# Performance work log

Hardware: AMD Instinct MI355X
Metric: run time of the kernel (lower is better)

The kernel has to match this reference:

```python
import jax, jax.numpy as jnp
import numpy as np

B, S, T = 8, 128, 24          # batch, src_len, max_len (enc_len = 2*S)
V, E, H = 32000, 512, 512     # vocab, embed_dim, hidden_dim
D = 3 * H + E                 # pointer-head feature dim = 2*dec_hid + emb + enc_hid


def setup_inputs() -> dict:
    key = jax.random.key(0)
    ks = jax.random.split(key, 25)
    def u(k, shape, scale):
        return jax.random.uniform(k, shape, jnp.float32, -scale, scale)
    s_h = 1.0 / np.sqrt(H).astype(np.float32)
    s_d = 1.0 / np.sqrt(D).astype(np.float32)
    s_2h = 1.0 / np.sqrt(2 * H).astype(np.float32)
    return {
        'pre_seq': jax.random.randint(ks[0], (B, S), 0, V),
        'post_seq': jax.random.randint(ks[1], (B, S), 0, V),
        'trg': jax.random.randint(ks[2], (B, T), 0, V),
        'emb': jax.random.normal(ks[3], (V, E), jnp.float32) * 0.02,
        'Wih_pre': u(ks[4], (3 * H, E), s_h), 'Whh_pre': u(ks[5], (3 * H, H), s_h),
        'bih_pre': u(ks[6], (3 * H,), s_h), 'bhh_pre': u(ks[7], (3 * H,), s_h),
        'Wih_post': u(ks[8], (3 * H, E), s_h), 'Whh_post': u(ks[9], (3 * H, H), s_h),
        'bih_post': u(ks[10], (3 * H,), s_h), 'bhh_post': u(ks[11], (3 * H,), s_h),
        'fc_enc_W': u(ks[12], (H, 2 * H), s_2h), 'fc_enc_b': u(ks[13], (H,), s_2h),
        'attn_W': u(ks[14], (H, 2 * H), s_2h), 'attn_b': u(ks[15], (H,), s_2h),
        'attn_v': u(ks[16], (1, H), s_h),
        'Wih_dec': u(ks[17], (3 * H, H + E), s_h), 'Whh_dec': u(ks[18], (3 * H, H), s_h),
        'bih_dec': u(ks[19], (3 * H,), s_h), 'bhh_dec': u(ks[20], (3 * H,), s_h),
        'fc_hid_W': u(ks[21], (D, D), s_d), 'fc_hid_b': u(ks[22], (D,), s_d),
        'fc_out_W': u(ks[23], (1, D), s_d), 'fc_out_b': u(ks[24], (1,), s_d),
    }


def gru_cell(x, h, Wih, Whh, bih, bhh):
    # torch GRU gate order: reset, update, new
    gi = x @ Wih.T + bih
    gh = h @ Whh.T + bhh
    ir, iz, inn = jnp.split(gi, 3, axis=-1)
    hr, hz, hn = jnp.split(gh, 3, axis=-1)
    r = jax.nn.sigmoid(ir + hr)
    z = jax.nn.sigmoid(iz + hz)
    n = jnp.tanh(inn + r * hn)
    return (1.0 - z) * n + z * h


def run_gru(x_seq, Wih, Whh, bih, bhh):
    # x_seq: [B, L, E] -> outputs [B, L, H], last hidden [B, H]
    h0 = jnp.zeros((x_seq.shape[0], Whh.shape[1]), x_seq.dtype)
    def step(h, x):
        h2 = gru_cell(x, h, Wih, Whh, bih, bhh)
        return h2, h2
    h_last, ys = jax.lax.scan(step, h0, jnp.swapaxes(x_seq, 0, 1))
    return jnp.swapaxes(ys, 0, 1), h_last


def reference(pre_seq, post_seq, trg, emb,
              Wih_pre, Whh_pre, bih_pre, bhh_pre,
              Wih_post, Whh_post, bih_post, bhh_post,
              fc_enc_W, fc_enc_b, attn_W, attn_b, attn_v,
              Wih_dec, Whh_dec, bih_dec, bhh_dec,
              fc_hid_W, fc_hid_b, fc_out_W, fc_out_b):
    bsz, src_len = pre_seq.shape
    # ---- Encoder (dropout in eval mode = identity) ----
    pre_out, pre_h = run_gru(emb[pre_seq], Wih_pre, Whh_pre, bih_pre, bhh_pre)
    post_out, post_h = run_gru(emb[post_seq], Wih_post, Whh_post, bih_post, bhh_post)
    enc_out = jnp.concatenate([pre_out, post_out], axis=1)          # [B, 2S, H]
    hidden = jnp.tanh(jnp.concatenate([pre_h, post_h], axis=-1) @ fc_enc_W.T + fc_enc_b)
    # ---- Attention: split attn_W into hidden- and encoder- parts (cat order: hidden, enc) ----
    W_hid, W_enc = attn_W[:, :H], attn_W[:, H:]
    enc_proj = jnp.einsum('blh,dh->bld', enc_out, W_enc) + attn_b   # step-invariant [B, L, H]
    L = enc_out.shape[1]
    # decoder input tokens: pre_seq[:, -1] then trg[:, :-1] (always teacher forced)
    tokens = jnp.concatenate([pre_seq[:, -1:], trg[:, :-1]], axis=1)  # [B, T]

    def dec_step(h, tok):
        e = emb[tok]                                                # [B, E]
        energy = jnp.tanh(enc_proj + (h @ W_hid.T)[:, None, :])     # [B, L, H]
        scores = jnp.einsum('blh,h->bl', energy, attn_v[0])
        a = jax.nn.softmax(scores, axis=1)                          # [B, L]
        weighted = jnp.einsum('bl,blh->bh', a, enc_out)             # [B, H]
        h2 = gru_cell(jnp.concatenate([e, weighted], axis=-1), h,
                      Wih_dec, Whh_dec, bih_dec, bhh_dec)           # [B, H]
        feats = jnp.concatenate([
            enc_out,
            jnp.broadcast_to(weighted[:, None, :], (bsz, L, H)),
            jnp.broadcast_to(h2[:, None, :], (bsz, L, H)),
            jnp.broadcast_to(e[:, None, :], (bsz, L, E)),
        ], axis=-1)                                                 # [B, L, 3H+E]
        hid = feats @ fc_hid_W.T + fc_hid_b                         # [B, L, D]
        logits = (hid @ fc_out_W.T + fc_out_b)[..., 0]              # [B, L]
        return h2, logits

    _, ys = jax.lax.scan(dec_step, hidden, tokens.T)                # [T, B, L]
    outs = jnp.swapaxes(ys, 0, 1)                                   # [B, T, L]
    return outs[:, :, :src_len], outs[:, :, src_len:]
```

## Files before the change

kernel.cpp:

```cpp
#include <hip/hip_runtime.h>
#include <cstdint>

#define B_ 8
#define S_ 128
#define T_ 24
#define E_ 512
#define H_ 512
#define H3_ 1536
#define L_ 256
#define D_ 2048

typedef unsigned long long u64;

__device__ __forceinline__ float fsig(float x) { return 1.0f / (1.0f + __expf(-x)); }
__device__ __forceinline__ float ftanh(float x) { return 1.0f - 2.0f / (1.0f + __expf(2.0f * x)); }
__device__ __forceinline__ float dot4(float4 a, float4 b) {
    return a.x * b.x + a.y * b.y + a.z * b.z + a.w * b.w;
}

__device__ __forceinline__ u64 cohLoadU64(const u64* p) {
    return __hip_atomic_load((u64*)p, __ATOMIC_RELAXED, __HIP_MEMORY_SCOPE_AGENT);
}
__device__ __forceinline__ void cohStoreU64(u64* p, u64 v) {
    __hip_atomic_store(p, v, __ATOMIC_RELAXED, __HIP_MEMORY_SCOPE_AGENT);
}
__device__ __forceinline__ float2 asF2(u64 v) { union { u64 u; float2 f; } x; x.u = v; return x.f; }
__device__ __forceinline__ u64 packF2(float v, float tag) { union { float2 f; u64 u; } x; x.f = make_float2(v, tag); return x.u; }

__global__ void k_boot(const int* __restrict__ pre, const int* __restrict__ post,
                       const int* __restrict__ trg,
                       int* __restrict__ idxPre, int* __restrict__ idxPost,
                       int* __restrict__ idxTok, float* __restrict__ wEff,
                       u64* __restrict__ clr, int n) {
    int gtid = blockIdx.x * 256 + threadIdx.x;
    for (int i = gtid; i < n; i += gridDim.x * 256) clr[i] = 0ull;
    if (gtid < 1024) {
        int s = gtid >> 3, b = gtid & 7;
        idxPre[gtid]  = pre[b * S_ + s];
        idxPost[gtid] = post[b * S_ + s];
    }
    if (gtid < T_ * B_) {
        int t = gtid >> 3, b = gtid & 7;
        idxTok[gtid] = (t == 0) ? pre[b * S_ + (S_ - 1)] : trg[b * T_ + (t - 1)];
    }
    if (gtid < 2048) wEff[gtid] = 0.f;
}

__device__ void gemm_body(
    const float* __restrict__ A, const int* __restrict__ Aidx, int lda,
    const float* __restrict__ Bm, int ldb,
    const float* __restrict__ bias, float* __restrict__ C,
    int N, int K, int gbx, int gby) {
    __shared__ float As[16][68];
    __shared__ float Bs[16][68];
    const int m0 = gbx * 64, n0 = gby * 64;
    const int tid = threadIdx.x;
    const int tm = tid >> 2;
    const int tk = (tid & 3) << 2;
    const int tx = tid & 15, ty = tid >> 4;
    const int am = m0 + tm;
    const float* Arow = A + (size_t)(Aidx ? Aidx[am] : am) * lda;
    const float* Brow = Bm + (size_t)(n0 + tm) * ldb;
    float acc[4][4] = {};
    for (int k0 = 0; k0 < K; k0 += 16) {
        float4 av = *(const float4*)(Arow + k0 + tk);
        float4 bv = *(const float4*)(Brow + k0 + tk);
        __syncthreads();
        As[tk][tm] = av.x; As[tk + 1][tm] = av.y; As[tk + 2][tm] = av.z; As[tk + 3][tm] = av.w;
        Bs[tk][tm] = bv.x; Bs[tk + 1][tm] = bv.y; Bs[tk + 2][tm] = bv.z; Bs[tk + 3][tm] = bv.w;
        __syncthreads();
#pragma unroll
        for (int k = 0; k < 16; ++k) {
            float4 a4 = *(const float4*)(&As[k][ty << 2]);
            float4 b4 = *(const float4*)(&Bs[k][tx << 2]);
            float ar[4] = {a4.x, a4.y, a4.z, a4.w};
            float br[4] = {b4.x, b4.y, b4.z, b4.w};
#pragma unroll
            for (int i = 0; i < 4; ++i)
#pragma unroll
                for (int j = 0; j < 4; ++j) acc[i][j] += ar[i] * br[j];
        }
    }
    float4 bb = bias ? *(const float4*)(bias + n0 + (tx << 2)) : make_float4(0.f, 0.f, 0.f, 0.f);
#pragma unroll
    for (int i = 0; i < 4; ++i) {
        int m = m0 + (ty << 2) + i;
        float4 o;
        o.x = acc[i][0] + bb.x; o.y = acc[i][1] + bb.y;
        o.z = acc[i][2] + bb.z; o.w = acc[i][3] + bb.w;
        *(float4*)(C + (size_t)m * N + n0 + (tx << 2)) = o;
    }
}

__global__ __launch_bounds__(256) void k_mid(
    const float* __restrict__ emb, const int* __restrict__ idxTok,
    const float* __restrict__ WihDec, const float* __restrict__ bihDec, float* __restrict__ giE,
    const float* __restrict__ encOut, const float* __restrict__ attnW,
    const float* __restrict__ attnB, float* __restrict__ encProj,
    const float* __restrict__ fcHidW, const float* __restrict__ fcHidB,
    const float* __restrict__ fcOutW, const float* __restrict__ fcOutB,
    float* __restrict__ wEff, float* __restrict__ bEff,
    const float* __restrict__ fcEncW, const float* __restrict__ fcEncB,
    float* __restrict__ hBuf) {
    const int bx = blockIdx.x;
    const int tid = threadIdx.x;
    if (bx < 72) {
        gemm_body(emb, idxTok, 512, WihDec, 1024, bihDec, giE, 1536, 512, bx % 3, bx / 3);
    } else if (bx < 328) {
        int r = bx - 72;
        gemm_body(encOut, nullptr, 512, attnW + 512, 1024, attnB, encProj, 512, 512, r & 31, r >> 5);
    } else if (bx < 457) {
        __shared__ float red[256];
        int wb = bx - 328;
        if (wb < 128) {
            int cblk = wb & 7, q = wb >> 3;
            int col = cblk * 256 + tid;
            int j0 = q * 128;
            float acc = 0.f;
            for (int j = j0; j < j0 + 128; ++j) acc += fcOutW[j] * fcHidW[(size_t)j * D_ + col];
            atomicAdd(wEff + col, acc);
        } else {
            float p = 0.f;
            for (int j = tid; j < D_; j += 256) p += fcOutW[j] * fcHidB[j];
            red[tid] = p;
            __syncthreads();
            for (int s = 128; s > 0; s >>= 1) {
                if (tid < s) red[tid] += red[tid + s];
                __syncthreads();
            }
            if (tid == 0) bEff[0] = red[0] + fcOutB[0];
        }
    } else {
        int o = (bx - 457) * 256 + tid;
        int b = o >> 9, j = o & 511;
        const float4* w4 = (const float4*)(fcEncW + (size_t)j * 1024);
        const float4* pre4 = (const float4*)(encOut + (((size_t)(b << 8) + 127) << 9));
        const float4* post4 = (const float4*)(encOut + (((size_t)(b << 8) + 255) << 9));
        float acc = fcEncB[j];
        for (int k = 0; k < 128; ++k) acc += dot4(w4[k], pre4[k]);
        for (int k = 0; k < 128; ++k) acc += dot4(w4[128 + k], post4[k]);
        hBuf[o] = ftanh(acc);
    }
}

__global__ __launch_bounds__(512, 2) void k_encoder(
    const float* __restrict__ emb, const int* __restrict__ idxPre, const int* __restrict__ idxPost,
    const float* __restrict__ WihPre, const float* __restrict__ WihPost,
    const float* __restrict__ bihPre, const float* __restrict__ bihPost,
    const float* __restrict__ WhhPre, const float* __restrict__ WhhPost,
    const float* __restrict__ bhhPre, const float* __restrict__ bhhPost,
    float* __restrict__ encOut, u64* __restrict__ encEx) {
    const int bx = blockIdx.x;
    const int chain = bx >> 4;
    const int p = bx & 15;
    const int gr = chain >> 3, b = chain & 7;
    const int kb = p << 5;
    const int tid = threadIdx.x;
    const int c = tid >> 4, l = tid & 15;
    const int j = kb + c;
    const float* Wih = gr ? WihPost : WihPre;
    const float* bih = gr ? bihPost : bihPre;
    const float* Whh = gr ? WhhPost : WhhPre;
    const float* bhh = gr ? bhhPost : bhhPre;
    const int* idx = gr ? idxPost : idxPre;
    u64* ex0 = encEx + chain * 512;

    __shared__ float hS[576];
    __shared__ float eS[576];

    float wr[32], wz[32], wn[32], ur[32], uz[32], un[32];
    {
        const float* r0 = Whh + (size_t)j * 512 + l * 32;
        const float* r1 = r0 + 512 * 512;
        const float* r2 = r1 + 512 * 512;
        const float* u0 = Wih + (size_t)j * 512 + l * 32;
        const float* u1 = u0 + 512 * 512;
        const float* u2 = u1 + 512 * 512;
#pragma unroll
        for (int m = 0; m < 32; ++m) {
            wr[m] = r0[m]; wz[m] = r1[m]; wn[m] = r2[m];
            ur[m] = u0[m]; uz[m] = u1[m]; un[m] = u2[m];
        }
    }
    const float b0 = bih[j] + bhh[j];
    const float b1 = bih[512 + j] + bhh[512 + j];
    const float bi2 = bih[1024 + j];
    const float bh2 = bhh[1024 + j];

    for (int t = 0; t < S_; ++t) {
        int tok = idx[t * 8 + b];
        float ev = emb[(size_t)tok * 512 + tid];
        if (t == 0) {
            hS[(tid >> 5) * 36 + (tid & 31)] = 0.f;
        } else {
            const float tag = (float)t;
            const u64* src = ex0 + (t & 1) * 8192;
            float v;
            for (;;) {
                float2 f = asF2(cohLoadU64(src + tid));
                if (f.y == tag) { v = f.x; break; }
                __builtin_amdgcn_s_sleep(1);
            }
            hS[(tid >> 5) * 36 + (tid & 31)] = v;
        }
        eS[(tid >> 5) * 36 + (tid & 31)] = ev;
        __syncthreads();
        const float* hseg = hS + l * 36;
        const float* eseg = eS + l * 36;
        float a0 = 0.f, a1 = 0.f, a2h = 0.f, a2i = 0.f;
#pragma unroll
        for (int m = 0; m < 32; ++m) {
            float hv = hseg[m], evv = eseg[m];
            a0 += wr[m] * hv + ur[m] * evv;
            a1 += wz[m] * hv + uz[m] * evv;
            a2h += wn[m] * hv;
            a2i += un[m] * evv;
        }
#pragma unroll
        for (int off = 8; off; off >>= 1) {
            a0 += __shfl_xor(a0, off, 16);
            a1 += __shfl_xor(a1, off, 16);
            a2h += __shfl_xor(a2h, off, 16);
            a2i += __shfl_xor(a2i, off, 16);
        }
        if (l == 0) {
            float r = fsig(a0 + b0);
            float z = fsig(a1 + b1);
            float n = ftanh(a2i + bi2 + r * (a2h + bh2));
            float h2 = (1.f - z) * n + z * hS[p * 36 + c];
            cohStoreU64(ex0 + ((t + 1) & 1) * 8192 + j, packF2(h2, (float)(t + 1)));
            encOut[(((size_t)(b << 8) + (gr << 7) + t) << 9) + j] = h2;
        }
        __syncthreads();
    }
}

__global__ __launch_bounds__(512, 2) void k_decoder(
    const float* __restrict__ encOut, const float* __restrict__ encProj,
    const float* __restrict__ attnW, const float* __restrict__ attnV,
    const float* __restrict__ WihDec, const float* __restrict__ WhhDec,
    const float* __restrict__ bhhDec, const float* __restrict__ giE,
    const float* __restrict__ wEff, const float* __restrict__ hBuf,
    const float* __restrict__ emb, const int* __restrict__ idxTok,
    u64* __restrict__ hEx, u64* __restrict__ hpP,
    u64* __restrict__ scEx, u64* __restrict__ wtEx,
    float* __restrict__ cpart, float* __restrict__ encDot, float* __restrict__ eDot4) {
    const int tid = threadIdx.x;
    const int bx = blockIdx.x;
    __shared__ float shm[9664];

    if (bx < 32) {
        const int g = bx;
        const int s = tid >> 5, kq = tid & 31;
        const int j = (g << 4) + s;
        float wr[16], wz[16], wn[16], vr[16], vz[16], vn[16], ap[16];
#pragma unroll
        for (int m = 0; m < 16; ++m) {
            int k = kq + 32 * m;
            wr[m] = WhhDec[(size_t)j * 512 + k];
            wz[m] = WhhDec[(size_t)(512 + j) * 512 + k];
            wn[m] = WhhDec[(size_t)(1024 + j) * 512 + k];
            vr[m] = WihDec[(size_t)j * 1024 + 512 + k];
            vz[m] = WihDec[(size_t)(512 + j) * 1024 + 512 + k];
            vn[m] = WihDec[(size_t)(1024 + j) * 1024 + 512 + k];
            ap[m] = attnW[(size_t)tid * 1024 + (g << 4) + m];
        }
        float* hL = shm;
        float* xL = shm + 4096;
        float* mS = shm + 8192;
        if (tid < 128) { int ss = tid >> 3, bb = tid & 7; mS[1152 + tid] = hBuf[(bb << 9) + (g << 4) + ss]; }
        if (tid < 48) mS[1280 + tid] = bhhDec[(tid >> 4) * 512 + (g << 4) + (tid & 15)];
        __syncthreads();
        {
            u64* hdst = hpP + (size_t)g * 4096;
#pragma unroll
            for (int bb = 0; bb < 8; ++bb) {
                float acch = 0.f;
#pragma unroll
                for (int m = 0; m < 16; ++m) acch += ap[m] * mS[1152 + m * 8 + bb];
                cohStoreU64(hdst + bb * 512 + tid, packF2(acch, 1.0f));
            }
        }
        for (int t = 0; t < T_; ++t) {
            const int par = t & 1;
            const float tagi = (float)(t + 1);
            if (t == 0) {
#pragma unroll
                for (int i = 0; i < 8; ++i) hL[tid + 512 * i] = hBuf[tid + 512 * i];
            } else {
                const float tagh = (float)t;
                const u64* src = hEx + par * 4096;
                float v[8];
                for (;;) {
                    u64 rr[8]; bool ok = true;
#pragma unroll
                    for (int i = 0; i < 8; ++i) rr[i] = cohLoadU64(src + tid + 512 * i);
#pragma unroll
                    for (int i = 0; i < 8; ++i) { float2 f = asF2(rr[i]); v[i] = f.x; ok &= (f.y == tagh); }
                    if (ok) break;
                    __builtin_amdgcn_s_sleep(1);
                }
#pragma unroll
                for (int i = 0; i < 8; ++i) hL[tid + 512 * i] = v[i];
            }
            __syncthreads();
            for (int bb = 0; bb < 8; ++bb) {
                const float* hb = hL + (bb << 9);
                float ar = 0.f, az = 0.f, an = 0.f;
#pragma unroll
                for (int m = 0; m < 16; ++m) {
                    float hv = hb[kq + 32 * m];
                    ar += wr[m] * hv; az += wz[m] * hv; an += wn[m] * hv;
                }
#pragma unroll
                for (int off = 16; off; off >>= 1) {
                    ar += __shfl_xor(ar, off); az += __shfl_xor(az, off); an += __shfl_xor(an, off);
                }
                if (kq == 0) {
                    mS[s * 8 + bb]       = ar;
                    mS[128 + s * 8 + bb] = az;
                    mS[256 + s * 8 + bb] = an;
                }
            }
            if (tid < 384) {
                int bb = tid / 48, idx2 = tid % 48, g3 = idx2 >> 4, ss = idx2 & 15;
                mS[768 + g3 * 128 + ss * 8 + bb] =
                    giE[((size_t)(t << 3) + bb) * H3_ + g3 * 512 + (g << 4) + ss];
            }
            {
                const u64* src = wtEx + par * 4096;
                float v[8];
                for (;;) {
                    u64 rr[8]; bool ok = true;
#pragma unroll
                    for (int i = 0; i < 8; ++i) rr[i] = cohLoadU64(src + tid + 512 * i);
#pragma unroll
                    for (int i = 0; i < 8; ++i) { float2 f = asF2(rr[i]); v[i] = f.x; ok &= (f.y == tagi); }
                    if (ok) break;
                    __builtin_amdgcn_s_sleep(1);
                }
#pragma unroll
                for (int i = 0; i < 8; ++i) xL[tid + 512 * i] = v[i];
            }
            __syncthreads();
            for (int bb = 0; bb < 8; ++bb) {
                const float* wb = xL + (bb << 9);
                float ar = 0.f, az = 0.f, an = 0.f;
#pragma unroll
                for (int m = 0; m < 16; ++m) {
                    float wv = wb[kq + 32 * m];
                    ar += vr[m] * wv; az += vz[m] * wv; an += vn[m] * wv;
                }
#pragma unroll
                for (int off = 16; off; off >>= 1) {
                    ar += __shfl_xor(ar, off); az += __shfl_xor(az, off); an += __shfl_xor(an, off);
                }
                if (kq == 0) {
                    mS[384 + s * 8 + bb] = ar;
                    mS[512 + s * 8 + bb] = az;
                    mS[640 + s * 8 + bb] = an;
                }
            }
            __syncthreads();
            if (tid < 128) {
                int ss = tid >> 3, bb = tid & 7;
                int jj = (g << 4) + ss;
                int o = ss * 8 + bb;
                float ghr = mS[o]       + mS[1280 + ss];
                float ghz = mS[128 + o] + mS[1296 + ss];
                float ghn = mS[256 + o] + mS[1312 + ss];
                float gir = mS[384 + o] + mS[768 + o];
                float giz = mS[512 + o] + mS[896 + o];
                float gin = mS[640 + o] + mS[1024 + o];
                float r = fsig(gir + ghr), z = fsig(giz + ghz);
                float n = ftanh(gin + r * ghn);
                float h2 = (1.f - z) * n + z * hL[(bb << 9) + jj];
                cohStoreU64(hEx + ((t + 1) & 1) * 4096 + (bb << 9) + jj, packF2(h2, (float)(t + 1)));
                mS[1152 + o] = h2;
                mS[1328 + o] = h2 * wEff[1024 + jj];
            }
            __syncthreads();
            if (tid < 8) {
                float pc = 0.f;
#pragma unroll
                for (int q = 0; q < 16; ++q) pc += mS[1328 + q * 8 + tid];
                cpart[(tid * T_ + t) * 48 + g] = pc;
            }
            if (t < T_ - 1) {
                const float tg = (float)(t + 2);
                u64* hdst = hpP + (size_t)((t + 1) & 1) * 131072 + (size_t)g * 4096;
#pragma unroll
                for (int bb = 0; bb < 8; ++bb) {
                    float acch = 0.f;
#pragma unroll
                    for (int m = 0; m < 16; ++m) acch += ap[m] * mS[1152 + m * 8 + bb];
                    cohStoreU64(hdst + bb * 512 + tid, packF2(acch, tg));
                }
            }
            __syncthreads();
        }
    } else if (bx < 96) {
        const int id = bx - 32;
        const int b = id >> 3, lq = id & 7;
        float* hpS = shm;
        float* vS  = shm + 512;
        vS[tid] = attnV[tid];
        __syncthreads();
        const int kq = tid & 63, lg = tid >> 6;
        for (int t = 0; t < T_; ++t) {
            const int par = t & 1;
            const float tagi = (float)(t + 1);
            {
                const u64* src = hpP + (size_t)par * 131072 + (size_t)b * 512 + tid;
                float sum;
                for (;;) {
                    bool ok = true; float s2 = 0.f;
                    u64 ra[16];
#pragma unroll
                    for (int pp = 0; pp < 16; ++pp) ra[pp] = cohLoadU64(src + (size_t)pp * 4096);
#pragma unroll
                    for (int pp = 0; pp < 16; ++pp) { float2 f = asF2(ra[pp]); s2 += f.x; ok &= (f.y == tagi); }
#pragma unroll
                    for (int pp = 0; pp < 16; ++pp) ra[pp] = cohLoadU64(src + (size_t)(16 + pp) * 4096);
#pragma unroll
                    for (int pp = 0; pp < 16; ++pp) { float2 f = asF2(ra[pp]); s2 += f.x; ok &= (f.y == tagi); }
                    if (ok) { sum = s2; break; }
                    __builtin_amdgcn_s_sleep(2);
                }
                hpS[tid] = sum;
            }
            __syncthreads();
            u64* dst = scEx + par * 2048 + (b << 8);
#pragma unroll
            for (int i = 0; i < 4; ++i) {
                int ll = lg + (i << 3);
                const float* ep = encProj + (((size_t)(b << 8) + (lq << 5) + ll) << 9);
                float sc = 0.f;
#pragma unroll
                for (int m = 0; m < 8; ++m) {
                    int k = kq + (m << 6);
                    sc += vS[k] * ftanh(ep[k] + hpS[k]);
                }
#pragma unroll
                for (int off = 32; off; off >>= 1) sc += __shfl_xor(sc, off);
                if (kq == 0) cohStoreU64(dst + (lq << 5) + ll, packF2(sc, tagi));
            }
            __syncthreads();
        }
    } else if (bx < 160) {
        const int id = bx - 96;
        const int b = id >> 3, cq = id & 7;
        const int c = tid & 63, lg = tid >> 6;
        float* aS = shm;
        float* rS = shm + 256;
        float* wS = shm + 288;
        float* lp = shm + 800;
        for (int t = 0; t < T_; ++t) {
            const int par = t & 1;
            const float tagi = (float)(t + 1);
            float sc = 0.f;
            if (tid < 256) {
                const u64* src = scEx + par * 2048 + (b << 8) + tid;
                for (;;) {
                    float2 f = asF2(cohLoadU64(src));
                    if (f.y == tagi) { sc = f.x; break; }
                    __builtin_amdgcn_s_sleep(1);
                }
            }
            float m = (tid < 256) ? sc : -1e30f;
#pragma unroll
            for (int off = 32; off; off >>= 1) m = fmaxf(m, __shfl_xor(m, off));
            if ((tid & 63) == 0) rS[tid >> 6] = m;
            __syncthreads();
            float mx = fmaxf(fmaxf(rS[0], rS[1]), fmaxf(rS[2], rS[3]));
            float e = (tid < 256) ? __expf(sc - mx) : 0.f;
            float ssum = e;
#pragma unroll
            for (int off = 32; off; off >>= 1) ssum += __shfl_xor(ssum, off);
            if ((tid & 63) == 0) rS[8 + (tid >> 6)] = ssum;
            if (tid < 256) aS[tid] = e;
            __syncthreads();
            float inv = 1.f / (rS[8] + rS[9] + rS[10] + rS[11]);
            float acc = 0.f;
#pragma unroll
            for (int mm = 0; mm < 32; ++mm) {
                int l = lg + (mm << 3);
                acc += aS[l] * encOut[(((size_t)(b << 8) + l) << 9) + (cq << 6) + c];
            }
            wS[lg * 64 + c] = acc;
            __syncthreads();
            if (tid < 64) {
                float wv = 0.f;
#pragma unroll
                for (int q = 0; q < 8; ++q) wv += wS[q * 64 + tid];
                wv *= inv;
                cohStoreU64(wtEx + par * 4096 + (b << 9) + (cq << 6) + tid, packF2(wv, tagi));
                lp[tid] = wv * wEff[512 + (cq << 6) + tid];
            }
            __syncthreads();
            if (tid == 0) {
                float pc = 0.f;
                for (int q = 0; q < 64; ++q) pc += lp[q];
                cpart[(b * T_ + t) * 48 + 32 + cq] = pc;
            }
            __syncthreads();
        }
    } else if (bx < 164) {
        int wid = tid >> 6, lane = tid & 63;
        int gw = (bx - 160) * 8 + wid;
        for (int o = gw; o < 2048; o += 32) {
            const float* row = encOut + ((size_t)o << 9);
            float s = 0.f;
            for (int k = lane; k < 512; k += 64) s += row[k] * wEff[k];
            for (int off = 32; off; off >>= 1) s += __shfl_down(s, off);
            if (lane == 0) encDot[o] = s;
        }
    } else {
        int wg = bx - 164;
        int o = wg * 8 + (tid >> 6);
        int lane = tid & 63;
        const float* row = emb + (size_t)idxTok[o] * E_;
        const float* w = wEff + 1536;
        float s = 0.f;
        for (int k = lane; k < 512; k += 64) s += row[k] * w[k];
        for (int off = 32; off; off >>= 1) s += __shfl_down(s, off);
        if (lane == 0) eDot4[o] = s;
    }
}

__global__ void k_csum(const float* __restrict__ cpart, const float* __restrict__ eDot4,
                       const float* __restrict__ bEff, float* __restrict__ cBuf) {
    int tid = threadIdx.x;
    if (tid < 192) {
        int b = tid / 24, t = tid % 24;
        float acc = eDot4[t * 8 + b] + bEff[0];
        const float* p = cpart + (b * T_ + t) * 48;
#pragma unroll
        for (int k = 0; k < 40; ++k) acc += p[k];
        cBuf[b * T_ + t] = acc;
    }
}

__global__ void k_final(const float* __restrict__ encDot, const float* __restrict__ c,
                        float* __restrict__ out) {
    int idx = blockIdx.x * 256 + threadIdx.x;
    const int half = B_ * T_ * S_;
    int w = idx < half ? idx : idx - half;
    int b = w / (T_ * S_);
    int r = w % (T_ * S_);
    int t = r / S_, sidx = r % S_;
    int l = (idx < half) ? sidx : (S_ + sidx);
    out[idx] = encDot[b * L_ + l] + c[b * T_ + t];
}

extern "C" void kernel_launch(void* const* d_in, const int* in_sizes, int n_in,
                              void* d_out, int out_size, void* d_ws, size_t ws_size,
                              hipStream_t stream) {
    const int* pre = (const int*)d_in[0];
    const int* post = (const int*)d_in[1];
    const int* trg = (const int*)d_in[2];
    const float* emb = (const float*)d_in[3];
    const float* WihPre = (const float*)d_in[4];
    const float* WhhPre = (const float*)d_in[5];
    const float* bihPre = (const float*)d_in[6];
    const float* bhhPre = (const float*)d_in[7];
    const float* WihPost = (const float*)d_in[8];
    const float* WhhPost = (const float*)d_in[9];
    const float* bihPost = (const float*)d_in[10];
    const float* bhhPost = (const float*)d_in[11];
    const float* fcEncW = (const float*)d_in[12];
    const float* fcEncB = (const float*)d_in[13];
    const float* attnW = (const float*)d_in[14];
    const float* attnB = (const float*)d_in[15];
    const float* attnV = (const float*)d_in[16];
    const float* WihDec = (const float*)d_in[17];
    const float* WhhDec = (const float*)d_in[18];
    const float* bihDec = (const float*)d_in[19];
    const float* bhhDec = (const float*)d_in[20];
    const float* fcHidW = (const float*)d_in[21];
    const float* fcHidB = (const float*)d_in[22];
    const float* fcOutW = (const float*)d_in[23];
    const float* fcOutB = (const float*)d_in[24];
    float* outp = (float*)d_out;

    float* base = (float*)d_ws;
    size_t off = 0;
    auto alloc = [&](size_t n) {
        float* p = base + off;
        off += (n + 63) & ~(size_t)63;
        return p;
    };
    float* giE = alloc(192 * 1536);
    float* encOut = alloc(8 * 256 * 512);
    float* encProj = alloc(8 * 256 * 512);
    float* wEff = alloc(2048);
    float* bEff = alloc(64);
    float* encDot = alloc(2048);
    float* eDot4 = alloc(256);
    float* hBuf = alloc(4096);
    float* cBuf = alloc(256);
    float* encExF = alloc(32768);
    float* hExF  = alloc(16384);
    float* hpPF  = alloc(524288);
    float* scExF = alloc(8192);
    float* wtExF = alloc(16384);
    float* cpart = alloc(8 * 24 * 48);
    int* idxPre = (int*)alloc(1024);
    int* idxPost = (int*)alloc(1024);
    int* idxTok = (int*)alloc(256);

    const int clearN = (32768 + 16384 + 524288 + 8192 + 16384) / 2;
    k_boot<<<512, 256, 0, stream>>>(pre, post, trg, idxPre, idxPost, idxTok, wEff,
                                    (u64*)encExF, clearN);
    k_encoder<<<256, 512, 0, stream>>>(emb, idxPre, idxPost, WihPre, WihPost,
                                       bihPre, bihPost, WhhPre, WhhPost,
                                       bhhPre, bhhPost, encOut, (u64*)encExF);
    k_mid<<<473, 256, 0, stream>>>(emb, idxTok, WihDec, bihDec, giE,
                                   encOut, attnW, attnB, encProj,
                                   fcHidW, fcHidB, fcOutW, fcOutB, wEff, bEff,
                                   fcEncW, fcEncB, hBuf);
    k_decoder<<<188, 512, 0, stream>>>(encOut, encProj, attnW, attnV,
                                       WihDec, WhhDec, bhhDec, giE, wEff, hBuf,
                                       emb, idxTok,
                                       (u64*)hExF, (u64*)hpPF, (u64*)scExF, (u64*)wtExF,
                                       cpart, encDot, eDot4);
    k_csum<<<1, 256, 0, stream>>>(cpart, eDot4, bEff, cBuf);
    k_final<<<192, 256, 0, stream>>>(encDot, cBuf, outp);
}
```

Measured before the change: 902.2 us.

## Replace per-element tagged exchanges with per-block flag counters in decoder

The decoder's cross-block exchanges for the hidden state, the attention-hidden projection partials and the weighted context used to pair every float with a step tag in 64-bit words. Consumers re-polled the whole buffer until every tag matched. Now the data is stored as plain floats, and each producer block publishes a single integer step counter after a block barrier. Consumers poll only the 32 or 64 counters, then read the data once. This halves exchange traffic and shrinks the boot-time buffer clearing. The catch is that correctness now relies on relaxed atomics plus workgroup barriers ordering data stores before flag stores, with no explicit release/acquire fences.

```diff
diff --git a/kernel.cpp b/kernel.cpp
--- a/kernel.cpp
+++ b/kernel.cpp
@@ -24,6 +24,18 @@
 __device__ __forceinline__ void cohStoreU64(u64* p, u64 v) {
     __hip_atomic_store(p, v, __ATOMIC_RELAXED, __HIP_MEMORY_SCOPE_AGENT);
 }
+__device__ __forceinline__ float cohLoadF(const float* p) {
+    return __hip_atomic_load((float*)p, __ATOMIC_RELAXED, __HIP_MEMORY_SCOPE_AGENT);
+}
+__device__ __forceinline__ void cohStoreF(float* p, float v) {
+    __hip_atomic_store(p, v, __ATOMIC_RELAXED, __HIP_MEMORY_SCOPE_AGENT);
+}
+__device__ __forceinline__ int cohLoadInt(const int* p) {
+    return __hip_atomic_load((int*)p, __ATOMIC_RELAXED, __HIP_MEMORY_SCOPE_AGENT);
+}
+__device__ __forceinline__ void cohStoreInt(int* p, int v) {
+    __hip_atomic_store(p, v, __ATOMIC_RELAXED, __HIP_MEMORY_SCOPE_AGENT);
+}
 __device__ __forceinline__ float2 asF2(u64 v) { union { u64 u; float2 f; } x; x.u = v; return x.f; }
 __device__ __forceinline__ u64 packF2(float v, float tag) { union { float2 f; u64 u; } x; x.f = make_float2(v, tag); return x.u; }
 
@@ -31,9 +43,10 @@
                        const int* __restrict__ trg,
                        int* __restrict__ idxPre, int* __restrict__ idxPost,
                        int* __restrict__ idxTok, float* __restrict__ wEff,
-                       u64* __restrict__ clr, int n) {
+                       u64* __restrict__ clr, int n, int* __restrict__ tags) {
     int gtid = blockIdx.x * 256 + threadIdx.x;
     for (int i = gtid; i < n; i += gridDim.x * 256) clr[i] = 0ull;
+    if (gtid < 128) tags[gtid] = 0;
     if (gtid < 1024) {
         int s = gtid >> 3, b = gtid & 7;
         idxPre[gtid]  = pre[b * S_ + s];
@@ -242,8 +255,9 @@
     const float* __restrict__ bhhDec, const float* __restrict__ giE,
     const float* __restrict__ wEff, const float* __restrict__ hBuf,
     const float* __restrict__ emb, const int* __restrict__ idxTok,
-    u64* __restrict__ hEx, u64* __restrict__ hpP,
-    u64* __restrict__ scEx, u64* __restrict__ wtEx,
+    float* __restrict__ hEx, float* __restrict__ hpD,
+    u64* __restrict__ scEx, float* __restrict__ wtEx,
+    int* __restrict__ gruTag, int* __restrict__ wtTag,
     float* __restrict__ cpart, float* __restrict__ encDot, float* __restrict__ eDot4) {
     const int tid = threadIdx.x;
     const int bx = blockIdx.x;
@@ -272,38 +286,37 @@
         if (tid < 48) mS[1280 + tid] = bhhDec[(tid >> 4) * 512 + (g << 4) + (tid & 15)];
         __syncthreads();
         {
-            u64* hdst = hpP + (size_t)g * 4096;
+            float* hdst = hpD + (size_t)g * 4096;
 #pragma unroll
             for (int bb = 0; bb < 8; ++bb) {
                 float acch = 0.f;
 #pragma unroll
                 for (int m = 0; m < 16; ++m) acch += ap[m] * mS[1152 + m * 8 + bb];
-                cohStoreU64(hdst + bb * 512 + tid, packF2(acch, 1.0f));
-            }
-        }
+                cohStoreF(hdst + bb * 512 + tid, acch);
+            }
+        }
+        __syncthreads();
+        if (tid == 0) cohStoreInt(gruTag + g, 1);
+
         for (int t = 0; t < T_; ++t) {
             const int par = t & 1;
-            const float tagi = (float)(t + 1);
             if (t == 0) {
 #pragma unroll
                 for (int i = 0; i < 8; ++i) hL[tid + 512 * i] = hBuf[tid + 512 * i];
+                __syncthreads();
             } else {
-                const float tagh = (float)t;
-                const u64* src = hEx + par * 4096;
-                float v[8];
+                const int want = t + 1;
                 for (;;) {
-                    u64 rr[8]; bool ok = true;
-#pragma unroll
-                    for (int i = 0; i < 8; ++i) rr[i] = cohLoadU64(src + tid + 512 * i);
-#pragma unroll
-                    for (int i = 0; i < 8; ++i) { float2 f = asF2(rr[i]); v[i] = f.x; ok &= (f.y == tagh); }
-                    if (ok) break;
-                    __builtin_amdgcn_s_sleep(1);
-                }
-#pragma unroll
-                for (int i = 0; i < 8; ++i) hL[tid + 512 * i] = v[i];
-            }
-            __syncthreads();
+                    int tg = want;
+                    if (tid < 32) tg = cohLoadInt(gruTag + tid);
+                    if (__syncthreads_and(tg >= want)) break;
+                    __builtin_amdgcn_s_sleep(2);
+                }
+                const float* src = hEx + par * 4096;
+#pragma unroll
+                for (int i = 0; i < 8; ++i) hL[tid + 512 * i] = cohLoadF(src + tid + 512 * i);
+                __syncthreads();
+            }
             for (int bb = 0; bb < 8; ++bb) {
                 const float* hb = hL + (bb << 9);
                 float ar = 0.f, az = 0.f, an = 0.f;
@@ -328,19 +341,16 @@
                     giE[((size_t)(t << 3) + bb) * H3_ + g3 * 512 + (g << 4) + ss];
             }
             {
-                const u64* src = wtEx + par * 4096;
-                float v[8];
+                const int want = t + 1;
                 for (;;) {
-                    u64 rr[8]; bool ok = true;
-#pragma unroll
-                    for (int i = 0; i < 8; ++i) rr[i] = cohLoadU64(src + tid + 512 * i);
-#pragma unroll
-                    for (int i = 0; i < 8; ++i) { float2 f = asF2(rr[i]); v[i] = f.x; ok &= (f.y == tagi); }
-                    if (ok) break;
-                    __builtin_amdgcn_s_sleep(1);
-                }
-#pragma unroll
-                for (int i = 0; i < 8; ++i) xL[tid + 512 * i] = v[i];
+                    int tg = want;
+                    if (tid < 64) tg = cohLoadInt(wtTag + tid);
+                    if (__syncthreads_and(tg >= want)) break;
+                    __builtin_amdgcn_s_sleep(2);
+                }
+                const float* src = wtEx + par * 4096;
+#pragma unroll
+                for (int i = 0; i < 8; ++i) xL[tid + 512 * i] = cohLoadF(src + tid + 512 * i);
             }
             __syncthreads();
             for (int bb = 0; bb < 8; ++bb) {
@@ -375,7 +385,7 @@
                 float r = fsig(gir + ghr), z = fsig(giz + ghz);
                 float n = ftanh(gin + r * ghn);
                 float h2 = (1.f - z) * n + z * hL[(bb << 9) + jj];
-                cohStoreU64(hEx + ((t + 1) & 1) * 4096 + (bb << 9) + jj, packF2(h2, (float)(t + 1)));
+                cohStoreF(hEx + ((t + 1) & 1) * 4096 + (bb << 9) + jj, h2);
                 mS[1152 + o] = h2;
                 mS[1328 + o] = h2 * wEff[1024 + jj];
             }
@@ -387,17 +397,17 @@
                 cpart[(tid * T_ + t) * 48 + g] = pc;
             }
             if (t < T_ - 1) {
-                const float tg = (float)(t + 2);
-                u64* hdst = hpP + (size_t)((t + 1) & 1) * 131072 + (size_t)g * 4096;
+                float* hdst = hpD + (size_t)((t + 1) & 1) * 131072 + (size_t)g * 4096;
 #pragma unroll
                 for (int bb = 0; bb < 8; ++bb) {
                     float acch = 0.f;
 #pragma unroll
                     for (int m = 0; m < 16; ++m) acch += ap[m] * mS[1152 + m * 8 + bb];
-                    cohStoreU64(hdst + bb * 512 + tid, packF2(acch, tg));
-                }
-            }
-            __syncthreads();
+                    cohStoreF(hdst + bb * 512 + tid, acch);
+                }
+                __syncthreads();
+                if (tid == 0) cohStoreInt(gruTag + g, t + 2);
+            }
         }
     } else if (bx < 96) {
         const int id = bx - 32;
@@ -411,22 +421,20 @@
             const int par = t & 1;
             const float tagi = (float)(t + 1);
             {
-                const u64* src = hpP + (size_t)par * 131072 + (size_t)b * 512 + tid;
-                float sum;
+                const int want = t + 1;
                 for (;;) {
-                    bool ok = true; float s2 = 0.f;
-                    u64 ra[16];
-#pragma unroll
-                    for (int pp = 0; pp < 16; ++pp) ra[pp] = cohLoadU64(src + (size_t)pp * 4096);
-#pragma unroll
-                    for (int pp = 0; pp < 16; ++pp) { float2 f = asF2(ra[pp]); s2 += f.x; ok &= (f.y == tagi); }
-#pragma unroll
-                    for (int pp = 0; pp < 16; ++pp) ra[pp] = cohLoadU64(src + (size_t)(16 + pp) * 4096);
-#pragma unroll
-                    for (int pp = 0; pp < 16; ++pp) { float2 f = asF2(ra[pp]); s2 += f.x; ok &= (f.y == tagi); }
-                    if (ok) { sum = s2; break; }
+                    int tg = want;
+                    if (tid < 32) tg = cohLoadInt(gruTag + tid);
+                    if (__syncthreads_and(tg >= want)) break;
                     __builtin_amdgcn_s_sleep(2);
                 }
+                const float* src = hpD + (size_t)par * 131072 + (size_t)b * 512 + tid;
+                float va[32];
+#pragma unroll
+                for (int g2 = 0; g2 < 32; ++g2) va[g2] = cohLoadF(src + (size_t)g2 * 4096);
+                float sum = 0.f;
+#pragma unroll
+                for (int g2 = 0; g2 < 32; ++g2) sum += va[g2];
                 hpS[tid] = sum;
             }
             __syncthreads();
@@ -494,11 +502,12 @@
 #pragma unroll
                 for (int q = 0; q < 8; ++q) wv += wS[q * 64 + tid];
                 wv *= inv;
-                cohStoreU64(wtEx + par * 4096 + (b << 9) + (cq << 6) + tid, packF2(wv, tagi));
+                cohStoreF(wtEx + par * 4096 + (b << 9) + (cq << 6) + tid, wv);
                 lp[tid] = wv * wEff[512 + (cq << 6) + tid];
             }
             __syncthreads();
             if (tid == 0) {
+                cohStoreInt(wtTag + (b << 3) + cq, t + 1);
                 float pc = 0.f;
                 for (int q = 0; q < 64; ++q) pc += lp[q];
                 cpart[(b * T_ + t) * 48 + 32 + cq] = pc;
@@ -600,18 +609,22 @@
     float* hBuf = alloc(4096);
     float* cBuf = alloc(256);
     float* encExF = alloc(32768);
-    float* hExF  = alloc(16384);
-    float* hpPF  = alloc(524288);
-    float* scExF = alloc(8192);
-    float* wtExF = alloc(16384);
+    float* scExF  = alloc(8192);
+    float* hExF  = alloc(8192);
+    float* hpDF  = alloc(262144);
+    float* wtExF = alloc(8192);
+    float* tagsF = alloc(128);
     float* cpart = alloc(8 * 24 * 48);
     int* idxPre = (int*)alloc(1024);
     int* idxPost = (int*)alloc(1024);
     int* idxTok = (int*)alloc(256);
 
-    const int clearN = (32768 + 16384 + 524288 + 8192 + 16384) / 2;
-    k_boot<<<512, 256, 0, stream>>>(pre, post, trg, idxPre, idxPost, idxTok, wEff,
-                                    (u64*)encExF, clearN);
+    int* gruTag = (int*)tagsF;
+    int* wtTag = gruTag + 32;
+
+    const int clearN = (32768 + 8192) / 2;
+    k_boot<<<128, 256, 0, stream>>>(pre, post, trg, idxPre, idxPost, idxTok, wEff,
+                                    (u64*)encExF, clearN, (int*)tagsF);
     k_encoder<<<256, 512, 0, stream>>>(emb, idxPre, idxPost, WihPre, WihPost,
                                        bihPre, bihPost, WhhPre, WhhPost,
                                        bhhPre, bhhPost, encOut, (u64*)encExF);
@@ -622,7 +635,8 @@
     k_decoder<<<188, 512, 0, stream>>>(encOut, encProj, attnW, attnV,
                                        WihDec, WhhDec, bhhDec, giE, wEff, hBuf,
                                        emb, idxTok,
-                                       (u64*)hExF, (u64*)hpPF, (u64*)scExF, (u64*)wtExF,
+                                       hExF, hpDF, (u64*)scExF, wtExF,
+                                       gruTag, wtTag,
                                        cpart, encDot, eDot4);
     k_csum<<<1, 256, 0, stream>>>(cpart, eDot4, bEff, cBuf);
     k_final<<<192, 256, 0, stream>>>(encDot, cBuf, outp);
```

Result: slower. 1.004 ms (+11.2%).

## Replace tagged partial-sum exchange with atomic accumulation and per-step counters

Applied to the files above, without the earlier changes.

Decoder GRU blocks now accumulate their attention hidden-projection partials directly into a per-timestep buffer with float atomic adds and bump a per-step arrival counter. Attention blocks poll one counter and read a single reduced value instead of loading and tag-checking 32 packed partials per element. This shrinks the exchange buffer and the boot-time clear, but adds contended L2 atomics, nondeterministic summation order, and relies on relaxed ordering between data adds and the counter.

```diff
diff --git a/kernel.cpp b/kernel.cpp
--- a/kernel.cpp
+++ b/kernel.cpp
@@ -23,6 +23,18 @@
 }
 __device__ __forceinline__ void cohStoreU64(u64* p, u64 v) {
     __hip_atomic_store(p, v, __ATOMIC_RELAXED, __HIP_MEMORY_SCOPE_AGENT);
+}
+__device__ __forceinline__ float cohLoadF(const float* p) {
+    return __hip_atomic_load((float*)p, __ATOMIC_RELAXED, __HIP_MEMORY_SCOPE_AGENT);
+}
+__device__ __forceinline__ void cohAddF(float* p, float v) {
+    __hip_atomic_fetch_add(p, v, __ATOMIC_RELAXED, __HIP_MEMORY_SCOPE_AGENT);
+}
+__device__ __forceinline__ int cohLoadInt(const int* p) {
+    return __hip_atomic_load((int*)p, __ATOMIC_RELAXED, __HIP_MEMORY_SCOPE_AGENT);
+}
+__device__ __forceinline__ void cohAddInt(int* p, int v) {
+    __hip_atomic_fetch_add(p, v, __ATOMIC_RELAXED, __HIP_MEMORY_SCOPE_AGENT);
 }
 __device__ __forceinline__ float2 asF2(u64 v) { union { u64 u; float2 f; } x; x.u = v; return x.f; }
 __device__ __forceinline__ u64 packF2(float v, float tag) { union { float2 f; u64 u; } x; x.f = make_float2(v, tag); return x.u; }
@@ -242,7 +254,7 @@
     const float* __restrict__ bhhDec, const float* __restrict__ giE,
     const float* __restrict__ wEff, const float* __restrict__ hBuf,
     const float* __restrict__ emb, const int* __restrict__ idxTok,
-    u64* __restrict__ hEx, u64* __restrict__ hpP,
+    u64* __restrict__ hEx, float* __restrict__ hpSum, int* __restrict__ hpCnt,
     u64* __restrict__ scEx, u64* __restrict__ wtEx,
     float* __restrict__ cpart, float* __restrict__ encDot, float* __restrict__ eDot4) {
     const int tid = threadIdx.x;
@@ -272,15 +284,17 @@
         if (tid < 48) mS[1280 + tid] = bhhDec[(tid >> 4) * 512 + (g << 4) + (tid & 15)];
         __syncthreads();
         {
-            u64* hdst = hpP + (size_t)g * 4096;
 #pragma unroll
             for (int bb = 0; bb < 8; ++bb) {
                 float acch = 0.f;
 #pragma unroll
                 for (int m = 0; m < 16; ++m) acch += ap[m] * mS[1152 + m * 8 + bb];
-                cohStoreU64(hdst + bb * 512 + tid, packF2(acch, 1.0f));
-            }
-        }
+                cohAddF(hpSum + (bb << 9) + tid, acch);
+            }
+        }
+        __syncthreads();
+        if (tid == 0) cohAddInt(hpCnt + 0, 1);
+
         for (int t = 0; t < T_; ++t) {
             const int par = t & 1;
             const float tagi = (float)(t + 1);
@@ -387,15 +401,16 @@
                 cpart[(tid * T_ + t) * 48 + g] = pc;
             }
             if (t < T_ - 1) {
-                const float tg = (float)(t + 2);
-                u64* hdst = hpP + (size_t)((t + 1) & 1) * 131072 + (size_t)g * 4096;
+                float* dst = hpSum + (size_t)(t + 1) * 4096;
 #pragma unroll
                 for (int bb = 0; bb < 8; ++bb) {
                     float acch = 0.f;
 #pragma unroll
                     for (int m = 0; m < 16; ++m) acch += ap[m] * mS[1152 + m * 8 + bb];
-                    cohStoreU64(hdst + bb * 512 + tid, packF2(acch, tg));
-                }
+                    cohAddF(dst + (bb << 9) + tid, acch);
+                }
+                __syncthreads();
+                if (tid == 0) cohAddInt(hpCnt + t + 1, 1);
             }
             __syncthreads();
         }
@@ -410,25 +425,11 @@
         for (int t = 0; t < T_; ++t) {
             const int par = t & 1;
             const float tagi = (float)(t + 1);
-            {
-                const u64* src = hpP + (size_t)par * 131072 + (size_t)b * 512 + tid;
-                float sum;
-                for (;;) {
-                    bool ok = true; float s2 = 0.f;
-                    u64 ra[16];
-#pragma unroll
-                    for (int pp = 0; pp < 16; ++pp) ra[pp] = cohLoadU64(src + (size_t)pp * 4096);
-#pragma unroll
-                    for (int pp = 0; pp < 16; ++pp) { float2 f = asF2(ra[pp]); s2 += f.x; ok &= (f.y == tagi); }
-#pragma unroll
-                    for (int pp = 0; pp < 16; ++pp) ra[pp] = cohLoadU64(src + (size_t)(16 + pp) * 4096);
-#pragma unroll
-                    for (int pp = 0; pp < 16; ++pp) { float2 f = asF2(ra[pp]); s2 += f.x; ok &= (f.y == tagi); }
-                    if (ok) { sum = s2; break; }
-                    __builtin_amdgcn_s_sleep(2);
-                }
-                hpS[tid] = sum;
-            }
+            for (;;) {
+                if (cohLoadInt(hpCnt + t) == 32) break;
+                __builtin_amdgcn_s_sleep(2);
+            }
+            hpS[tid] = cohLoadF(hpSum + (size_t)t * 4096 + (b << 9) + tid);
             __syncthreads();
             u64* dst = scEx + par * 2048 + (b << 8);
 #pragma unroll
@@ -600,17 +601,18 @@
     float* hBuf = alloc(4096);
     float* cBuf = alloc(256);
     float* encExF = alloc(32768);
-    float* hExF  = alloc(16384);
-    float* hpPF  = alloc(524288);
-    float* scExF = alloc(8192);
-    float* wtExF = alloc(16384);
+    float* hExF   = alloc(16384);
+    float* scExF  = alloc(8192);
+    float* wtExF  = alloc(16384);
+    float* hpSumF = alloc(98304);
+    float* hpCntF = alloc(64);
     float* cpart = alloc(8 * 24 * 48);
     int* idxPre = (int*)alloc(1024);
     int* idxPost = (int*)alloc(1024);
     int* idxTok = (int*)alloc(256);
 
-    const int clearN = (32768 + 16384 + 524288 + 8192 + 16384) / 2;
-    k_boot<<<512, 256, 0, stream>>>(pre, post, trg, idxPre, idxPost, idxTok, wEff,
+    const int clearN = (32768 + 16384 + 8192 + 16384 + 98304 + 64) / 2;
+    k_boot<<<128, 256, 0, stream>>>(pre, post, trg, idxPre, idxPost, idxTok, wEff,
                                     (u64*)encExF, clearN);
     k_encoder<<<256, 512, 0, stream>>>(emb, idxPre, idxPost, WihPre, WihPost,
                                        bihPre, bihPost, WhhPre, WhhPost,
@@ -622,7 +624,8 @@
     k_decoder<<<188, 512, 0, stream>>>(encOut, encProj, attnW, attnV,
                                        WihDec, WhhDec, bhhDec, giE, wEff, hBuf,
                                        emb, idxTok,
-                                       (u64*)hExF, (u64*)hpPF, (u64*)scExF, (u64*)wtExF,
+                                       (u64*)hExF, hpSumF, (int*)hpCntF,
+                                       (u64*)scExF, (u64*)wtExF,
                                        cpart, encDot, eDot4);
     k_csum<<<1, 256, 0, stream>>>(cpart, eDot4, bEff, cBuf);
     k_final<<<192, 256, 0, stream>>>(encDot, cBuf, outp);
```

Result: slower. 921.3 us (+2.1%).
